# Optimization experiments

Measured on AMD Instinct MI355X. Metric: run time of the kernel, lower is better.

Reference implementation:

```python
import jax, jax.numpy as jnp
import numpy as np

B, N = 1, 384          # batch, N_res
C_Z, C_H, H = 128, 32, 4  # pair channels, per-head hidden, heads
INF = 1.0e9
LN_EPS = 1e-5


def setup_inputs() -> dict:
    key = jax.random.key(0)
    ks = jax.random.split(key, 8)
    s = lambda k, shape: jax.random.normal(k, shape, jnp.float32) * 0.02
    return {
        "z": jax.random.normal(ks[0], (B, N, N, C_Z), jnp.float32),
        "mask": jnp.ones((B, N, N), jnp.float32),
        "ln_gamma": jnp.ones((C_Z,), jnp.float32),
        "ln_beta": jnp.zeros((C_Z,), jnp.float32),
        "w_bias": s(ks[1], (C_Z, H)),          # Linear(c_z, num_heads, bias=False)
        "w_q": s(ks[2], (C_Z, H * C_H)),        # no-bias q/k/v projections
        "w_k": s(ks[3], (C_Z, H * C_H)),
        "w_v": s(ks[4], (C_Z, H * C_H)),
        "w_g": s(ks[5], (C_Z, H * C_H)),        # gating projection
        "b_g": jnp.ones((H * C_H,), jnp.float32),  # gating bias init ones
        "w_o": s(ks[6], (H * C_H, C_Z)),        # output projection
        "b_o": jnp.zeros((C_Z,), jnp.float32),
    }


def reference(z, mask, ln_gamma, ln_beta, w_bias, w_q, w_k, w_v, w_g, b_g, w_o, b_o):
    # ta_type == "starting": no transposes.
    # LayerNorm over c_z
    mu = jnp.mean(z, axis=-1, keepdims=True)
    var = jnp.var(z, axis=-1, keepdims=True)
    zn = (z - mu) * jax.lax.rsqrt(var + LN_EPS) * ln_gamma + ln_beta  # [B,N,N,C_Z]

    # triangle bias: linear(z) -> [B,N,N,H] -> movedim -> [B,H,i,j], broadcast over batch-row axis
    tri_bias = jnp.einsum('bijc,ch->bhij', zn, w_bias)  # [B,H,N,N]
    # mask bias: masked keys get -inf; mask shape [B,i,k] broadcast to [B,i,1,1,k]
    mask_bias = INF * (mask - 1.0)

    wq = w_q.reshape(C_Z, H, C_H)
    wk = w_k.reshape(C_Z, H, C_H)
    wv = w_v.reshape(C_Z, H, C_H)
    q = jnp.einsum('bijc,chd->bijhd', zn, wq) * (C_H ** -0.5)  # scale q
    k = jnp.einsum('bijc,chd->bijhd', zn, wk)
    v = jnp.einsum('bijc,chd->bijhd', zn, wv)

    # attention over the j/k axis per row i: logits [B,i,H,j,k]
    logits = jnp.einsum('bijhd,bikhd->bihjk', q, k)
    logits = logits + mask_bias[:, :, None, None, :] + tri_bias[:, None, :, :, :]
    a = jax.nn.softmax(logits, axis=-1)
    o = jnp.einsum('bihjk,bikhd->bijhd', a, v)  # [B,N,N,H,C_H]

    # gating
    g = jax.nn.sigmoid(jnp.einsum('bijc,ce->bije', zn, w_g) + b_g)  # [B,N,N,H*C_H]
    o = o.reshape(B, N, N, H * C_H) * g
    return jnp.einsum('bije,ec->bijc', o, w_o) + b_o  # [B,N,N,C_Z]
```

## Files before the change

### kernel.cpp

```cpp
#include <hip/hip_runtime.h>

#define NRES 384
#define CZ 128
#define NH 4
#define CH 32
#define NN (NRES * NRES)
#define NNCZ ((size_t)NN * CZ)

typedef unsigned short u16;
typedef __attribute__((ext_vector_type(4))) unsigned short us4;
typedef __attribute__((ext_vector_type(8))) unsigned short us8;
typedef __attribute__((ext_vector_type(8))) short s8;
typedef __attribute__((ext_vector_type(4))) float f4;

__device__ __forceinline__ float bf2f(u16 u) {
  return __uint_as_float(((unsigned)u) << 16);
}
__device__ __forceinline__ u16 f2bf(float f) {
  unsigned u = __float_as_uint(f);
  u += 0x7fffu + ((u >> 16) & 1u);
  return (u16)(u >> 16);
}

template<bool F32>
__device__ __forceinline__ float ld1(const void* p, size_t i) {
  if constexpr (F32) return ((const float*)p)[i];
  else return bf2f(((const u16*)p)[i]);
}

template<bool F32>
__device__ __forceinline__ void ld4v(const void* p, size_t i, float o[4]) {
  if constexpr (F32) {
    const float4 a = *(const float4*)((const float*)p + i);
    o[0] = a.x; o[1] = a.y; o[2] = a.z; o[3] = a.w;
  } else {
    const us4 v = *(const us4*)((const u16*)p + i);
    #pragma unroll
    for (int u = 0; u < 4; ++u) o[u] = bf2f(v[u]);
  }
}

template<bool F32>
__device__ __forceinline__ void ld8(const void* p, size_t i, float o[8]) {
  if constexpr (F32) {
    const float4 a = *(const float4*)((const float*)p + i);
    const float4 b = *(const float4*)((const float*)p + i + 4);
    o[0] = a.x; o[1] = a.y; o[2] = a.z; o[3] = a.w;
    o[4] = b.x; o[5] = b.y; o[6] = b.z; o[7] = b.w;
  } else {
    const us8 v = *(const us8*)((const u16*)p + i);
    #pragma unroll
    for (int u = 0; u < 8; ++u) o[u] = bf2f(v[u]);
  }
}

__global__ void k_probe(const u16* __restrict__ z, int* __restrict__ flag) {
  int weird = 0;
  for (int i = threadIdx.x; i < 256; i += 64) {
    const int e = (z[i] >> 7) & 0xFF;
    if (e < 0x70 || e > 0x8F) weird++;
  }
  #pragma unroll
  for (int m = 1; m < 64; m <<= 1) weird += __shfl_xor(weird, m, 64);
  if (threadIdx.x == 0) *flag = (weird >= 16) ? 1 : 0;
}

template<bool F32>
__global__ __launch_bounds__(256, 2) void k_ln_proj(
    const void* __restrict__ z, const void* __restrict__ gma, const void* __restrict__ bta,
    const void* __restrict__ wbias, const void* __restrict__ wq, const void* __restrict__ wk,
    const void* __restrict__ wv, const void* __restrict__ wg, const void* __restrict__ bg,
    u16* __restrict__ qb, u16* __restrict__ kb, u16* __restrict__ vb, u16* __restrict__ gb,
    float* __restrict__ triT, const int* __restrict__ flag)
{
  if ((*flag != 0) != F32) return;
  __shared__ __align__(16) u16 znl[128 * 136];
  __shared__ __align__(16) u16 WT[CZ * CZ];
  const int t = threadIdx.x;
  const int lane = t & 63;
  const int wid = t >> 6;
  const int n16 = lane & 15;
  const int quad = lane >> 4;
  const int rowBase = blockIdx.x * 128;

  const int c0 = n16 * 8;
  float g8[8], b8[8];
  ld8<F32>(gma, c0, g8);
  ld8<F32>(bta, c0, b8);
  for (int it = 0; it < 8; ++it) {
    const int rl = wid * 32 + it * 4 + quad;
    float x[8];
    ld8<F32>(z, (size_t)(rowBase + rl) * CZ + c0, x);
    float s = 0.f, q2 = 0.f;
    #pragma unroll
    for (int u = 0; u < 8; ++u) { s += x[u]; q2 += x[u] * x[u]; }
    #pragma unroll
    for (int m = 1; m < 16; m <<= 1) {
      s  += __shfl_xor(s, m, 64);
      q2 += __shfl_xor(q2, m, 64);
    }
    const float mu = s * (1.0f / CZ);
    const float rs = rsqrtf(q2 * (1.0f / CZ) - mu * mu + 1e-5f);
    us8 o;
    #pragma unroll
    for (int u = 0; u < 8; ++u) o[u] = f2bf((x[u] - mu) * rs * g8[u] + b8[u]);
    *(us8*)&znl[rl * 136 + c0] = o;
  }
  __syncthreads();

  float wb4[8][4];
  #pragma unroll
  for (int cc = 0; cc < 8; ++cc) ld4v<F32>(wbias, (size_t)(c0 + cc) * NH, wb4[cc]);
  for (int it = 0; it < 8; ++it) {
    const int rl = wid * 32 + it * 4 + quad;
    const us8 zv8 = *(const us8*)&znl[rl * 136 + c0];
    float a0 = 0.f, a1 = 0.f, a2 = 0.f, a3 = 0.f;
    #pragma unroll
    for (int cc = 0; cc < 8; ++cc) {
      const float zv = bf2f(zv8[cc]);
      a0 += zv * wb4[cc][0]; a1 += zv * wb4[cc][1];
      a2 += zv * wb4[cc][2]; a3 += zv * wb4[cc][3];
    }
    #pragma unroll
    for (int m = 1; m < 16; m <<= 1) {
      a0 += __shfl_xor(a0, m, 64); a1 += __shfl_xor(a1, m, 64);
      a2 += __shfl_xor(a2, m, 64); a3 += __shfl_xor(a3, m, 64);
    }
    if (n16 < 4) {
      const float v = (n16 == 0) ? a0 : (n16 == 1) ? a1 : (n16 == 2) ? a2 : a3;
      const int P = rowBase + rl;
      const int aI = P / NRES, bI = P % NRES;
      triT[(size_t)n16 * NN + (size_t)bI * NRES + aI] = v;
    }
  }

  const u16 scl_q = 1;
  for (int arr = 0; arr < 4; ++arr) {
    const void* W = (arr == 0) ? wq : (arr == 1) ? wk : (arr == 2) ? wv : wg;
    __syncthreads();
    #pragma unroll
    for (int it = 0; it < 16; ++it) {
      const int c = (t >> 5) + it * 8;
      const int m0 = (t & 31) * 4;
      float w4[4];
      ld4v<F32>(W, (size_t)c * CZ + m0, w4);
      const int ks = c >> 5, qq = (c >> 3) & 3, j = c & 7;
      #pragma unroll
      for (int mm = 0; mm < 4; ++mm) {
        const int m = m0 + mm;
        WT[ks * 4096 + (((m >> 4) * 4 + qq) * 16 + (m & 15)) * 8 + j] = f2bf(w4[mm]);
      }
    }
    __syncthreads();

    f4 acc[2][8];
    #pragma unroll
    for (int i = 0; i < 2; ++i)
      #pragma unroll
      for (int nt = 0; nt < 8; ++nt) acc[i][nt] = f4{0.f, 0.f, 0.f, 0.f};

    #pragma unroll
    for (int ks = 0; ks < 4; ++ks) {
      s8 a[2], b[8];
      #pragma unroll
      for (int i = 0; i < 2; ++i)
        a[i] = *(const s8*)&WT[ks * 4096 + (((wid * 2 + i) * 4 + quad) * 16 + n16) * 8];
      #pragma unroll
      for (int nt = 0; nt < 8; ++nt)
        b[nt] = *(const s8*)&znl[(nt * 16 + n16) * 136 + ks * 32 + quad * 8];
      #pragma unroll
      for (int i = 0; i < 2; ++i)
        #pragma unroll
        for (int nt = 0; nt < 8; ++nt)
          acc[i][nt] = __builtin_amdgcn_mfma_f32_16x16x32_bf16(a[i], b[nt], acc[i][nt], 0, 0, 0);
    }

    u16* dstb = (arr == 0) ? qb : (arr == 1) ? kb : (arr == 2) ? vb : gb;
    #pragma unroll
    for (int i = 0; i < 2; ++i) {
      const int mt = wid * 2 + i;
      const int och0 = mt * 16 + quad * 4;
      float e4[4];
      if (arr == 3) ld4v<F32>(bg, och0, e4);
      #pragma unroll
      for (int nt = 0; nt < 8; ++nt) {
        us4 o;
        #pragma unroll
        for (int r = 0; r < 4; ++r) {
          float v = acc[i][nt][r];
          if (arr == 0) v *= 0.17677669529663687f;
          else if (arr == 3) v = 1.0f / (1.0f + __expf(-(v + e4[r])));
          o[r] = f2bf(v);
        }
        *(us4*)&dstb[(size_t)(rowBase + nt * 16 + n16) * CZ + och0] = o;
      }
    }
  }
  (void)scl_q;
}

template<bool F32>
__global__ __launch_bounds__(256, 3) void k_attn(
    const u16* __restrict__ qb, const u16* __restrict__ kb, const u16* __restrict__ vb,
    const u16* __restrict__ gb, const float* __restrict__ triT, const void* __restrict__ msk,
    u16* __restrict__ ogb, const int* __restrict__ flag)
{
  if ((*flag != 0) != F32) return;
  __shared__ __align__(16) u16 KB[24 * 4 * 16 * 8];
  __shared__ __align__(16) u16 VB[12 * 4 * 32 * 8];
  __shared__ __align__(16) u16 Pch[4][16 * 40];
  const int t = threadIdx.x;
  const int i = blockIdx.x >> 2;
  const int h = blockIdx.x & 3;
  const size_t base_i = (size_t)i * NRES;

  #pragma unroll
  for (int it = 0; it < 12; ++it) {
    const int idx = t + it * 256;
    const int kk = idx >> 3;
    const int d0 = (idx & 7) * 4;
    const size_t off = (base_i + kk) * CZ + h * CH + d0;
    const us4 kv = *(const us4*)&kb[off];
    const int tt = kk >> 4, nn = kk & 15, qq = d0 >> 3, jb = d0 & 7;
    *(us4*)&KB[((tt * 4 + qq) * 16 + nn) * 8 + jb] = kv;
    const us4 vv = *(const us4*)&vb[off];
    const int cc = kk >> 5, q2 = (kk >> 3) & 3, jj = kk & 7;
    u16* vdst = &VB[((cc * 4 + q2) * 32 + d0) * 8 + jj];
    vdst[0] = vv[0]; vdst[8] = vv[1]; vdst[16] = vv[2]; vdst[24] = vv[3];
  }
  __syncthreads();

  const int wid = t >> 6;
  const int lane = t & 63;
  const int n = lane & 15;
  const int quad = lane >> 4;
  const float* trih = triT + (size_t)h * NN;
  u16* pb = &Pch[wid][0];

  float mb[24];
  #pragma unroll
  for (int tt = 0; tt < 24; ++tt)
    mb[tt] = 1.0e9f * (ld1<F32>(msk, base_i + tt * 16 + n) - 1.0f);

  for (int jt = wid; jt < 24; jt += 4) {
    const int jrow0 = jt * 16;
    const s8 aq = *(const s8*)&qb[(base_i + jrow0 + n) * CZ + h * CH + quad * 8];

    f4 S[24];
    #pragma unroll
    for (int tt = 0; tt < 24; ++tt) {
      const s8 bk = *(const s8*)&KB[((tt * 4 + quad) * 16 + n) * 8];
      const f4 z4 = {0.f, 0.f, 0.f, 0.f};
      S[tt] = __builtin_amdgcn_mfma_f32_16x16x32_bf16(aq, bk, z4, 0, 0, 0);
    }
    #pragma unroll
    for (int tt = 0; tt < 24; ++tt) {
      const float4 t4 = *(const float4*)&trih[(size_t)(tt * 16 + n) * NRES + jrow0 + quad * 4];
      S[tt][0] += t4.x + mb[tt];
      S[tt][1] += t4.y + mb[tt];
      S[tt][2] += t4.z + mb[tt];
      S[tt][3] += t4.w + mb[tt];
    }
    f4 mx = S[0];
    #pragma unroll
    for (int tt = 1; tt < 24; ++tt) {
      #pragma unroll
      for (int r = 0; r < 4; ++r) mx[r] = fmaxf(mx[r], S[tt][r]);
    }
    #pragma unroll
    for (int s = 1; s < 16; s <<= 1) {
      #pragma unroll
      for (int r = 0; r < 4; ++r) mx[r] = fmaxf(mx[r], __shfl_xor(mx[r], s, 64));
    }
    f4 sum = {0.f, 0.f, 0.f, 0.f};
    #pragma unroll
    for (int tt = 0; tt < 24; ++tt) {
      #pragma unroll
      for (int r = 0; r < 4; ++r) {
        S[tt][r] = __expf(S[tt][r] - mx[r]);
        sum[r] += S[tt][r];
      }
    }
    #pragma unroll
    for (int s = 1; s < 16; s <<= 1) {
      #pragma unroll
      for (int r = 0; r < 4; ++r) sum[r] += __shfl_xor(sum[r], s, 64);
    }
    f4 inv;
    #pragma unroll
    for (int r = 0; r < 4; ++r) inv[r] = 1.0f / sum[r];

    f4 O0 = {0.f, 0.f, 0.f, 0.f}, O1 = {0.f, 0.f, 0.f, 0.f};
    #pragma unroll
    for (int c = 0; c < 12; ++c) {
      #pragma unroll
      for (int half = 0; half < 2; ++half) {
        const int tt = 2 * c + half;
        #pragma unroll
        for (int r = 0; r < 4; ++r)
          pb[(quad * 4 + r) * 40 + half * 16 + n] = f2bf(S[tt][r]);
      }
      const s8 ap  = *(const s8*)&pb[n * 40 + quad * 8];
      const s8 bv0 = *(const s8*)&VB[((c * 4 + quad) * 32 + n) * 8];
      const s8 bv1 = *(const s8*)&VB[((c * 4 + quad) * 32 + 16 + n) * 8];
      O0 = __builtin_amdgcn_mfma_f32_16x16x32_bf16(ap, bv0, O0, 0, 0, 0);
      O1 = __builtin_amdgcn_mfma_f32_16x16x32_bf16(ap, bv1, O1, 0, 0, 0);
    }
    #pragma unroll
    for (int r = 0; r < 4; ++r) {
      const size_t rowoff = (base_i + jrow0 + quad * 4 + r) * CZ + h * CH;
      const float iv = inv[r];
      const float g0 = bf2f(gb[rowoff + n]);
      const float g1 = bf2f(gb[rowoff + 16 + n]);
      ogb[rowoff + n]      = f2bf(O0[r] * iv * g0);
      ogb[rowoff + 16 + n] = f2bf(O1[r] * iv * g1);
    }
  }
}

template<bool F32>
__global__ __launch_bounds__(256, 2) void k_out(
    const u16* __restrict__ og, const void* __restrict__ wo, const void* __restrict__ bo,
    void* __restrict__ outp, const int* __restrict__ flag)
{
  if ((*flag != 0) != F32) return;
  __shared__ __align__(16) u16 ol[128 * 136];
  __shared__ __align__(16) u16 WT[CZ * CZ];
  const int t = threadIdx.x;
  const int lane = t & 63;
  const int wid = t >> 6;
  const int n16 = lane & 15;
  const int quad = lane >> 4;
  const int rowBase = blockIdx.x * 128;

  #pragma unroll
  for (int it = 0; it < 8; ++it) {
    const int idx8 = t + it * 256;
    const int r = idx8 >> 4;
    const int c0 = (idx8 & 15) * 8;
    *(us8*)&ol[r * 136 + c0] = *(const us8*)&og[(size_t)(rowBase + r) * CZ + c0];
  }
  #pragma unroll
  for (int it = 0; it < 16; ++it) {
    const int c = (t >> 5) + it * 8;
    const int m0 = (t & 31) * 4;
    float w4[4];
    ld4v<F32>(wo, (size_t)c * CZ + m0, w4);
    const int ks = c >> 5, qq = (c >> 3) & 3, j = c & 7;
    #pragma unroll
    for (int mm = 0; mm < 4; ++mm) {
      const int m = m0 + mm;
      WT[ks * 4096 + (((m >> 4) * 4 + qq) * 16 + (m & 15)) * 8 + j] = f2bf(w4[mm]);
    }
  }
  __syncthreads();

  f4 acc[2][8];
  #pragma unroll
  for (int i = 0; i < 2; ++i)
    #pragma unroll
    for (int nt = 0; nt < 8; ++nt) acc[i][nt] = f4{0.f, 0.f, 0.f, 0.f};

  #pragma unroll
  for (int ks = 0; ks < 4; ++ks) {
    s8 a[2], b[8];
    #pragma unroll
    for (int i = 0; i < 2; ++i)
      a[i] = *(const s8*)&WT[ks * 4096 + (((wid * 2 + i) * 4 + quad) * 16 + n16) * 8];
    #pragma unroll
    for (int nt = 0; nt < 8; ++nt)
      b[nt] = *(const s8*)&ol[(nt * 16 + n16) * 136 + ks * 32 + quad * 8];
    #pragma unroll
    for (int i = 0; i < 2; ++i)
      #pragma unroll
      for (int nt = 0; nt < 8; ++nt)
        acc[i][nt] = __builtin_amdgcn_mfma_f32_16x16x32_bf16(a[i], b[nt], acc[i][nt], 0, 0, 0);
  }

  #pragma unroll
  for (int i = 0; i < 2; ++i) {
    const int och0 = (wid * 2 + i) * 16 + quad * 4;
    float b4[4];
    ld4v<F32>(bo, och0, b4);
    #pragma unroll
    for (int nt = 0; nt < 8; ++nt) {
      const size_t off = (size_t)(rowBase + nt * 16 + n16) * CZ + och0;
      if constexpr (F32) {
        float4 o;
        o.x = acc[i][nt][0] + b4[0]; o.y = acc[i][nt][1] + b4[1];
        o.z = acc[i][nt][2] + b4[2]; o.w = acc[i][nt][3] + b4[3];
        *(float4*)&((float*)outp)[off] = o;
      } else {
        us4 o;
        #pragma unroll
        for (int r = 0; r < 4; ++r) o[r] = f2bf(acc[i][nt][r] + b4[r]);
        *(us4*)&((u16*)outp)[off] = o;
      }
    }
  }
}

extern "C" void kernel_launch(void* const* d_in, const int* in_sizes, int n_in,
                              void* d_out, int out_size, void* d_ws, size_t ws_size,
                              hipStream_t stream) {
  const void* z     = d_in[0];
  const void* msk   = d_in[1];
  const void* gma   = d_in[2];
  const void* bta   = d_in[3];
  const void* wbias = d_in[4];
  const void* wq    = d_in[5];
  const void* wk    = d_in[6];
  const void* wv    = d_in[7];
  const void* wg    = d_in[8];
  const void* bg    = d_in[9];
  const void* wo    = d_in[10];
  const void* bo    = d_in[11];

  char* ws = (char*)d_ws;
  int* flag = (int*)ws;
  u16* qb = (u16*)(ws + 256);
  u16* kb = qb + NNCZ;
  u16* vb = kb + NNCZ;
  u16* gb = vb + NNCZ;
  float* triT = (float*)(gb + NNCZ);
  u16* ogb = qb;

  k_probe<<<dim3(1), dim3(64), 0, stream>>>((const u16*)z, flag);

  k_ln_proj<false><<<dim3(NN / 128), dim3(256), 0, stream>>>(
      z, gma, bta, wbias, wq, wk, wv, wg, bg, qb, kb, vb, gb, triT, flag);
  k_ln_proj<true><<<dim3(NN / 128), dim3(256), 0, stream>>>(
      z, gma, bta, wbias, wq, wk, wv, wg, bg, qb, kb, vb, gb, triT, flag);

  k_attn<false><<<dim3(NRES * NH), dim3(256), 0, stream>>>(
      qb, kb, vb, gb, triT, msk, ogb, flag);
  k_attn<true><<<dim3(NRES * NH), dim3(256), 0, stream>>>(
      qb, kb, vb, gb, triT, msk, ogb, flag);

  k_out<false><<<dim3(NN / 128), dim3(256), 0, stream>>>(ogb, wo, bo, d_out, flag);
  k_out<true><<<dim3(NN / 128), dim3(256), 0, stream>>>(ogb, wo, bo, d_out, flag);
}
```

Measured before the change: 514.0 us.

## Use online softmax over key chunks in attention to cut registers and LDS

```diff
diff --git a/kernel.cpp b/kernel.cpp
--- a/kernel.cpp
+++ b/kernel.cpp
@@ -200,15 +200,15 @@
 }
 
 template<bool F32>
-__global__ __launch_bounds__(256, 3) void k_attn(
+__global__ __launch_bounds__(256, 4) void k_attn(
     const u16* __restrict__ qb, const u16* __restrict__ kb, const u16* __restrict__ vb,
     const u16* __restrict__ gb, const float* __restrict__ triT, const void* __restrict__ msk,
     u16* __restrict__ ogb, const int* __restrict__ flag)
 {
   if ((*flag != 0) != F32) return;
-  __shared__ __align__(16) u16 KB[24 * 4 * 16 * 8];
   __shared__ __align__(16) u16 VB[12 * 4 * 32 * 8];
   __shared__ __align__(16) u16 Pch[4][16 * 40];
+  __shared__ __align__(16) float mbL[NRES];
   const int t = threadIdx.x;
   const int i = blockIdx.x >> 2;
   const int h = blockIdx.x & 3;
@@ -219,15 +219,15 @@
     const int idx = t + it * 256;
     const int kk = idx >> 3;
     const int d0 = (idx & 7) * 4;
-    const size_t off = (base_i + kk) * CZ + h * CH + d0;
-    const us4 kv = *(const us4*)&kb[off];
-    const int tt = kk >> 4, nn = kk & 15, qq = d0 >> 3, jb = d0 & 7;
-    *(us4*)&KB[((tt * 4 + qq) * 16 + nn) * 8 + jb] = kv;
-    const us4 vv = *(const us4*)&vb[off];
-    const int cc = kk >> 5, q2 = (kk >> 3) & 3, jj = kk & 7;
-    u16* vdst = &VB[((cc * 4 + q2) * 32 + d0) * 8 + jj];
+    const us4 vv = *(const us4*)&vb[(base_i + kk) * CZ + h * CH + d0];
+    const int cc2 = kk >> 5;
+    const int kap = kk & 31;
+    const int p = 2 * (kap & 15) + (kap >> 4);
+    u16* vdst = &VB[((cc2 * 4 + (p >> 3)) * 32 + d0) * 8 + (p & 7)];
     vdst[0] = vv[0]; vdst[8] = vv[1]; vdst[16] = vv[2]; vdst[24] = vv[3];
   }
+  for (int idx = t; idx < NRES; idx += 256)
+    mbL[idx] = 1.0e9f * (ld1<F32>(msk, base_i + idx) - 1.0f);
   __syncthreads();
 
   const int wid = t >> 6;
@@ -237,75 +237,91 @@
   const float* trih = triT + (size_t)h * NN;
   u16* pb = &Pch[wid][0];
 
-  float mb[24];
-  #pragma unroll
-  for (int tt = 0; tt < 24; ++tt)
-    mb[tt] = 1.0e9f * (ld1<F32>(msk, base_i + tt * 16 + n) - 1.0f);
-
   for (int jt = wid; jt < 24; jt += 4) {
     const int jrow0 = jt * 16;
     const s8 aq = *(const s8*)&qb[(base_i + jrow0 + n) * CZ + h * CH + quad * 8];
 
-    f4 S[24];
-    #pragma unroll
-    for (int tt = 0; tt < 24; ++tt) {
-      const s8 bk = *(const s8*)&KB[((tt * 4 + quad) * 16 + n) * 8];
-      const f4 z4 = {0.f, 0.f, 0.f, 0.f};
-      S[tt] = __builtin_amdgcn_mfma_f32_16x16x32_bf16(aq, bk, z4, 0, 0, 0);
-    }
-    #pragma unroll
-    for (int tt = 0; tt < 24; ++tt) {
-      const float4 t4 = *(const float4*)&trih[(size_t)(tt * 16 + n) * NRES + jrow0 + quad * 4];
-      S[tt][0] += t4.x + mb[tt];
-      S[tt][1] += t4.y + mb[tt];
-      S[tt][2] += t4.z + mb[tt];
-      S[tt][3] += t4.w + mb[tt];
-    }
-    f4 mx = S[0];
-    #pragma unroll
-    for (int tt = 1; tt < 24; ++tt) {
-      #pragma unroll
-      for (int r = 0; r < 4; ++r) mx[r] = fmaxf(mx[r], S[tt][r]);
-    }
-    #pragma unroll
-    for (int s = 1; s < 16; s <<= 1) {
-      #pragma unroll
-      for (int r = 0; r < 4; ++r) mx[r] = fmaxf(mx[r], __shfl_xor(mx[r], s, 64));
-    }
-    f4 sum = {0.f, 0.f, 0.f, 0.f};
-    #pragma unroll
-    for (int tt = 0; tt < 24; ++tt) {
+    f4 O0 = {0.f, 0.f, 0.f, 0.f}, O1 = {0.f, 0.f, 0.f, 0.f};
+    f4 l4 = {0.f, 0.f, 0.f, 0.f};
+    f4 m4 = {-1.0e30f, -1.0e30f, -1.0e30f, -1.0e30f};
+
+    #pragma unroll 1
+    for (int cc = 0; cc < 4; ++cc) {
+      f4 S[6];
+      #pragma unroll
+      for (int u = 0; u < 6; ++u) {
+        const int tt = cc * 6 + u;
+        const s8 bk = *(const s8*)&kb[(base_i + tt * 16 + n) * CZ + h * CH + quad * 8];
+        const f4 z4 = {0.f, 0.f, 0.f, 0.f};
+        S[u] = __builtin_amdgcn_mfma_f32_16x16x32_bf16(aq, bk, z4, 0, 0, 0);
+      }
+      #pragma unroll
+      for (int u = 0; u < 6; ++u) {
+        const int tt = cc * 6 + u;
+        const float mbv = mbL[tt * 16 + n];
+        const float4 t4 = *(const float4*)&trih[(size_t)(tt * 16 + n) * NRES + jrow0 + quad * 4];
+        S[u][0] += t4.x + mbv;
+        S[u][1] += t4.y + mbv;
+        S[u][2] += t4.z + mbv;
+        S[u][3] += t4.w + mbv;
+      }
+      f4 mx = S[0];
+      #pragma unroll
+      for (int u = 1; u < 6; ++u) {
+        #pragma unroll
+        for (int r = 0; r < 4; ++r) mx[r] = fmaxf(mx[r], S[u][r]);
+      }
+      #pragma unroll
+      for (int sft = 1; sft < 16; sft <<= 1) {
+        #pragma unroll
+        for (int r = 0; r < 4; ++r) mx[r] = fmaxf(mx[r], __shfl_xor(mx[r], sft, 64));
+      }
+      f4 sc;
       #pragma unroll
       for (int r = 0; r < 4; ++r) {
-        S[tt][r] = __expf(S[tt][r] - mx[r]);
-        sum[r] += S[tt][r];
-      }
-    }
-    #pragma unroll
-    for (int s = 1; s < 16; s <<= 1) {
-      #pragma unroll
-      for (int r = 0; r < 4; ++r) sum[r] += __shfl_xor(sum[r], s, 64);
+        const float mn = fmaxf(m4[r], mx[r]);
+        sc[r] = __expf(m4[r] - mn);
+        m4[r] = mn;
+      }
+      #pragma unroll
+      for (int r = 0; r < 4; ++r) {
+        O0[r] *= sc[r]; O1[r] *= sc[r]; l4[r] *= sc[r];
+      }
+      #pragma unroll
+      for (int u = 0; u < 6; ++u) {
+        #pragma unroll
+        for (int r = 0; r < 4; ++r) {
+          S[u][r] = __expf(S[u][r] - m4[r]);
+          l4[r] += S[u][r];
+        }
+      }
+      #pragma unroll
+      for (int s = 0; s < 3; ++s) {
+        #pragma unroll
+        for (int r = 0; r < 4; ++r) {
+          const unsigned w = (unsigned)f2bf(S[2 * s][r]) |
+                             ((unsigned)f2bf(S[2 * s + 1][r]) << 16);
+          *(unsigned*)&pb[(quad * 4 + r) * 40 + n * 2] = w;
+        }
+        const int C = cc * 3 + s;
+        const s8 ap  = *(const s8*)&pb[n * 40 + quad * 8];
+        const s8 bv0 = *(const s8*)&VB[((C * 4 + quad) * 32 + n) * 8];
+        const s8 bv1 = *(const s8*)&VB[((C * 4 + quad) * 32 + 16 + n) * 8];
+        O0 = __builtin_amdgcn_mfma_f32_16x16x32_bf16(ap, bv0, O0, 0, 0, 0);
+        O1 = __builtin_amdgcn_mfma_f32_16x16x32_bf16(ap, bv1, O1, 0, 0, 0);
+      }
+    }
+
+    f4 sum = l4;
+    #pragma unroll
+    for (int sft = 1; sft < 16; sft <<= 1) {
+      #pragma unroll
+      for (int r = 0; r < 4; ++r) sum[r] += __shfl_xor(sum[r], sft, 64);
     }
     f4 inv;
     #pragma unroll
     for (int r = 0; r < 4; ++r) inv[r] = 1.0f / sum[r];
 
-    f4 O0 = {0.f, 0.f, 0.f, 0.f}, O1 = {0.f, 0.f, 0.f, 0.f};
-    #pragma unroll
-    for (int c = 0; c < 12; ++c) {
-      #pragma unroll
-      for (int half = 0; half < 2; ++half) {
-        const int tt = 2 * c + half;
-        #pragma unroll
-        for (int r = 0; r < 4; ++r)
-          pb[(quad * 4 + r) * 40 + half * 16 + n] = f2bf(S[tt][r]);
-      }
-      const s8 ap  = *(const s8*)&pb[n * 40 + quad * 8];
-      const s8 bv0 = *(const s8*)&VB[((c * 4 + quad) * 32 + n) * 8];
-      const s8 bv1 = *(const s8*)&VB[((c * 4 + quad) * 32 + 16 + n) * 8];
-      O0 = __builtin_amdgcn_mfma_f32_16x16x32_bf16(ap, bv0, O0, 0, 0, 0);
-      O1 = __builtin_amdgcn_mfma_f32_16x16x32_bf16(ap, bv1, O1, 0, 0, 0);
-    }
     #pragma unroll
     for (int r = 0; r < 4; ++r) {
       const size_t rowoff = (base_i + jrow0 + quad * 4 + r) * CZ + h * CH;
```

Result: slower. 532.8 us (+3.6%).
